# Kernel tuning notes

Measured on AMD Instinct MI355X. Metric: run time of the kernel, lower is better.

## Reference

```python
import jax, jax.numpy as jnp
import numpy as np

D = 1024
S = 2048
B = 4


def setup_inputs() -> dict:
    key = jax.random.key(0)
    ks = jax.random.split(key, 9)
    sc = 1.0 / np.sqrt(D)
    return {
        "x": jax.random.normal(ks[0], (B, S, D), dtype=jnp.float32),
        "Wq": jax.random.normal(ks[1], (D, D), dtype=jnp.float32) * sc,
        "bq": jax.random.normal(ks[2], (D,), dtype=jnp.float32) * 0.02,
        "Wk": jax.random.normal(ks[3], (D, D), dtype=jnp.float32) * sc,
        "bk": jax.random.normal(ks[4], (D,), dtype=jnp.float32) * 0.02,
        "Wv": jax.random.normal(ks[5], (D, D), dtype=jnp.float32) * sc,
        "bv": jax.random.normal(ks[6], (D,), dtype=jnp.float32) * 0.02,
        "Wp": jax.random.normal(ks[7], (D, D), dtype=jnp.float32) * sc,
        "bp": jax.random.normal(ks[8], (D,), dtype=jnp.float32) * 0.02,
    }


def reference(x, Wq, bq, Wk, bk, Wv, bv, Wp, bp):
    # torch nn.Linear: y = x @ W.T + b  (W stored [out, in])
    q = jnp.einsum("bsd,ed->bse", x, Wq) + bq  # [B,S,D]
    k = jnp.einsum("bsd,ed->bse", x, Wk) + bk
    v = jnp.einsum("bsd,ed->bse", x, Wv) + bv

    scale = 1.0 / jnp.sqrt(jnp.asarray(q.shape[-1], q.dtype))
    # single-head attention: contract over full embd_dim (no head split in source)
    scores = jnp.einsum("bqd,bkd->bqk", q, k) * scale  # [B,S,S]

    seq = x.shape[1]
    causal = jnp.tril(jnp.ones((seq, seq), dtype=bool))  # [S,S]
    scores = jnp.where(causal[None, :, :], scores, -jnp.inf)

    attn = jax.nn.softmax(scores, axis=-1)  # [B,S,S]
    out = jnp.einsum("bqk,bkd->bqd", attn, v)  # [B,S,D]
    out = jnp.einsum("bsd,ed->bse", out, Wp) + bp
    return out
```

## Files before the change

### kernel.cpp

```cpp
#include <hip/hip_runtime.h>

#define AS1(p) ((const __attribute__((address_space(1))) void*)(p))
#define AS3(p) ((__attribute__((address_space(3))) void*)(p))

typedef unsigned short u16;
typedef __bf16 bf16x8 __attribute__((ext_vector_type(8)));
typedef short s16x8 __attribute__((ext_vector_type(8)));
typedef float f32x4 __attribute__((ext_vector_type(4)));
typedef unsigned short u16x4 __attribute__((ext_vector_type(4)));
typedef unsigned short u16x8v __attribute__((ext_vector_type(8)));

__device__ __forceinline__ u16 f2bf(float x) {
    unsigned u = __float_as_uint(x);
    unsigned r = (u + 0x7FFFu + ((u >> 16) & 1u)) >> 16;
    return (u16)r;
}
__device__ __forceinline__ float bf2f(u16 x) {
    return __uint_as_float(((unsigned)x) << 16);
}

template <typename V8>
__device__ __forceinline__ auto mfma_sel(V8 a, V8 b, f32x4 c, int)
    -> decltype(__builtin_amdgcn_mfma_f32_16x16x32_bf16(a, b, c, 0, 0, 0))
{
    return __builtin_amdgcn_mfma_f32_16x16x32_bf16(a, b, c, 0, 0, 0);
}
template <typename V8>
__device__ __forceinline__ f32x4 mfma_sel(V8 a, V8 b, f32x4 c, long)
{
    s16x8 a2 = __builtin_bit_cast(s16x8, a);
    s16x8 b2 = __builtin_bit_cast(s16x8, b);
    return __builtin_amdgcn_mfma_f32_16x16x32_bf16(a2, b2, c, 0, 0, 0);
}
__device__ __forceinline__ f32x4 mfma16x16x32(bf16x8 a, bf16x8 b, f32x4 c)
{
    return mfma_sel(a, b, c, 0);
}

__global__ __launch_bounds__(256) void cvt_bf16_kernel(const float* __restrict__ in,
                                                       u16* __restrict__ out, int n4)
{
    int i = blockIdx.x * 256 + threadIdx.x;
    if (i >= n4) return;
    float4 f = ((const float4*)in)[i];
    u16x4 o;
    o.x = f2bf(f.x); o.y = f2bf(f.y); o.z = f2bf(f.z); o.w = f2bf(f.w);
    ((u16x4*)out)[i] = o;
}

__global__ __launch_bounds__(256) void cvt_w4_kernel(const float* __restrict__ Wq,
                                                     const float* __restrict__ Wk,
                                                     const float* __restrict__ Wv,
                                                     const float* __restrict__ Wp,
                                                     u16* __restrict__ Wcat,
                                                     u16* __restrict__ Wpb, int n4)
{
    int i = blockIdx.x * 256 + threadIdx.x;
    if (i >= n4) return;
    const int by = blockIdx.y;
    const float* src = (by == 0) ? Wq : (by == 1) ? Wk : (by == 2) ? Wv : Wp;
    u16* dst = (by == 3) ? Wpb : (Wcat + (size_t)by * n4 * 4);
    float4 f = ((const float4*)src)[i];
    u16x4 o;
    o.x = f2bf(f.x); o.y = f2bf(f.y); o.z = f2bf(f.z); o.w = f2bf(f.w);
    ((u16x4*)dst)[i] = o;
}

__global__ __launch_bounds__(256) void transpose16(const u16* __restrict__ in,
                                                   u16* __restrict__ out, int R, int C)
{
    __shared__ u16 tl[64][65];
    const int tr0 = blockIdx.y * 64, tc0 = blockIdx.x * 64;
    const int t = threadIdx.x;
    const int r = t >> 2, c4 = (t & 3) << 4;

    const u16* src = in + (size_t)(tr0 + r) * C + tc0 + c4;
    u16x8v a0 = *(const u16x8v*)src;
    u16x8v a1 = *(const u16x8v*)(src + 8);
    #pragma unroll
    for (int j = 0; j < 8; ++j) { tl[r][c4 + j] = a0[j]; tl[r][c4 + 8 + j] = a1[j]; }
    __syncthreads();

    u16x8v b0, b1;
    #pragma unroll
    for (int j = 0; j < 8; ++j) { b0[j] = tl[c4 + j][r]; b1[j] = tl[c4 + 8 + j][r]; }
    u16* dst = out + (size_t)(tc0 + r) * R + tr0 + c4;
    *(u16x8v*)dst = b0;
    *(u16x8v*)(dst + 8) = b1;
}

#define GBM 128
#define GBN 256
#define GBK 64
#define ABUF 16384
#define BBUF 32768
#define TBUF (ABUF + BBUF)
#define LDS_NT2 (3 * TBUF)

template <int BIAS, int OUTBF16, int CSKIP, int CKB>
__global__ __launch_bounds__(512, 2)
void gemm_nt2(const u16* __restrict__ A, const u16* __restrict__ B,
              void* __restrict__ Cv, const float* __restrict__ bias,
              void* __restrict__ C2, const float* __restrict__ bias2,
              void* __restrict__ C3, const float* __restrict__ bias3,
              int M, int N, int K, int lda, int ldb, int ldc,
              long long sA, long long sB, long long sC, float scale)
{
    extern __shared__ char smem[];

    int by = blockIdx.y;
    if (CKB) by = gridDim.y - 1 - by;
    const int m0 = by * GBM;
    const int n0 = blockIdx.x * GBN;
    if (CSKIP && n0 > m0 + GBM - 1) return;

    const int z = blockIdx.z;
    A += (size_t)z * (size_t)sA;
    B += (size_t)z * (size_t)sB;

    const int t = threadIdx.x;
    const int lane = t & 63;
    const int w = t >> 6;
    const int wr = w >> 2;
    const int wc = w & 3;
    const int fr = lane & 15, fg = lane >> 4;

    int Keff = K;
    if (CKB) { Keff = m0 + GBM; if (Keff > K) Keff = K; }
    const int nk = Keff / GBK;

    f32x4 acc[4][4] = {};

    auto STAGE = [&](int kt, int buf) {
        const int k0 = kt * GBK;
        char* sb = smem + buf * TBUF;
        #pragma unroll
        for (int i = 0; i < 2; ++i) {
            int c = t + i * 512;
            int row = c >> 3;
            int sl = (c & 7) ^ (row & 7);
            __builtin_amdgcn_global_load_lds(
                AS1(A + (size_t)(m0 + row) * lda + k0 + sl * 8),
                AS3(sb + c * 16), 16, 0, 0);
        }
        #pragma unroll
        for (int i = 0; i < 4; ++i) {
            int c = t + i * 512;
            int row = c >> 3;
            int sl = (c & 7) ^ (row & 7);
            __builtin_amdgcn_global_load_lds(
                AS1(B + (size_t)(n0 + row) * ldb + k0 + sl * 8),
                AS3(sb + ABUF + c * 16), 16, 0, 0);
        }
    };

    STAGE(0, 0);
    STAGE(1, 1);
    asm volatile("s_waitcnt vmcnt(6)" ::: "memory");
    __builtin_amdgcn_s_barrier();

    int cur = 0;
    for (int kt = 0; kt < nk; ++kt) {
        int pb = cur + 2; if (pb >= 3) pb -= 3;
        const bool pf = (kt + 2 < nk);
        if (pf) STAGE(kt + 2, pb);

        const char* la = smem + cur * TBUF;
        const char* lb = la + ABUF;
        #pragma unroll
        for (int kk = 0; kk < GBK; kk += 32) {
            const int cs = (kk >> 3) + fg;
            bf16x8 af[4], bfv[4];
            #pragma unroll
            for (int mi = 0; mi < 4; ++mi) {
                int row = wr * 64 + mi * 16 + fr;
                af[mi] = *(const bf16x8*)(la + (row << 7) + ((cs ^ (row & 7)) << 4));
            }
            #pragma unroll
            for (int ni = 0; ni < 4; ++ni) {
                int row = wc * 64 + ni * 16 + fr;
                bfv[ni] = *(const bf16x8*)(lb + (row << 7) + ((cs ^ (row & 7)) << 4));
            }
            __builtin_amdgcn_s_setprio(1);
            #pragma unroll
            for (int mi = 0; mi < 4; ++mi)
                #pragma unroll
                for (int ni = 0; ni < 4; ++ni)
                    acc[mi][ni] = mfma16x16x32(af[mi], bfv[ni], acc[mi][ni]);
            __builtin_amdgcn_s_setprio(0);
        }

        if (pf) asm volatile("s_waitcnt vmcnt(6)" ::: "memory");
        else    asm volatile("s_waitcnt vmcnt(0)" ::: "memory");
        __builtin_amdgcn_s_barrier();
        ++cur; if (cur >= 3) cur = 0;
    }

    #pragma unroll
    for (int mi = 0; mi < 4; ++mi) {
        #pragma unroll
        for (int ni = 0; ni < 4; ++ni) {
            int col = n0 + wc * 64 + ni * 16 + fr;
            int row0 = m0 + wr * 64 + mi * 16 + fg * 4;
            if (BIAS == 3) {
                int seg = col >> 10;
                int ccol = col & 1023;
                u16* dst = (seg == 0) ? (u16*)Cv : (seg == 1) ? (u16*)C2 : (u16*)C3;
                float b = ((seg == 0) ? bias : (seg == 1) ? bias2 : bias3)[ccol];
                float sc_ = (seg == 0) ? scale : 1.f;
                #pragma unroll
                for (int j = 0; j < 4; ++j)
                    dst[(size_t)(row0 + j) * 1024 + ccol] =
                        f2bf((acc[mi][ni][j] + b) * sc_);
            } else {
                float bval = (BIAS == 1) ? bias[col] : 0.f;
                #pragma unroll
                for (int j = 0; j < 4; ++j) {
                    float v = (acc[mi][ni][j] + bval) * scale;
                    size_t off = (size_t)z * (size_t)sC + (size_t)(row0 + j) * ldc + col;
                    if (OUTBF16) ((u16*)Cv)[off] = f2bf(v);
                    else         ((float*)Cv)[off] = v;
                }
            }
        }
    }
}

__device__ __forceinline__ float waveMax(float v) {
    #pragma unroll
    for (int o = 32; o > 0; o >>= 1) v = fmaxf(v, __shfl_xor(v, o));
    return v;
}
__device__ __forceinline__ float waveSum(float v) {
    #pragma unroll
    for (int o = 32; o > 0; o >>= 1) v += __shfl_xor(v, o);
    return v;
}

__global__ __launch_bounds__(256) void softmax_causal_bf16(u16* __restrict__ scores, int S)
{
    __shared__ float red[4];
    const int gb = blockIdx.x;
    const int b = gb / S;
    const int i = gb - b * S;
    u16* row = scores + (size_t)b * S * S + (size_t)i * S;
    const int t = threadIdx.x;
    const int jlim = ((i >> 7) + 1) << 7;
    const int j0 = t << 3;
    const bool act = j0 < jlim;

    float v[8];
    float mx = -1e30f;
    if (act) {
        u16x8v raw = *(const u16x8v*)(row + j0);
        #pragma unroll
        for (int e = 0; e < 8; ++e) {
            float x = bf2f(raw[e]);
            v[e] = (j0 + e <= i) ? x : -1e30f;
            mx = fmaxf(mx, v[e]);
        }
    } else {
        #pragma unroll
        for (int e = 0; e < 8; ++e) v[e] = -1e30f;
    }

    mx = waveMax(mx);
    const int wv = t >> 6;
    if ((t & 63) == 0) red[wv] = mx;
    __syncthreads();
    mx = fmaxf(fmaxf(red[0], red[1]), fmaxf(red[2], red[3]));
    __syncthreads();

    float sum = 0.f;
    if (act) {
        #pragma unroll
        for (int e = 0; e < 8; ++e) {
            float ex = (v[e] > -1e29f) ? __expf(v[e] - mx) : 0.f;
            v[e] = ex;
            sum += ex;
        }
    }
    sum = waveSum(sum);
    if ((t & 63) == 0) red[wv] = sum;
    __syncthreads();
    sum = red[0] + red[1] + red[2] + red[3];
    const float inv = 1.f / sum;

    if (act) {
        u16x8v o;
        #pragma unroll
        for (int e = 0; e < 8; ++e) o[e] = f2bf(v[e] * inv);
        *(u16x8v*)(row + j0) = o;
    }
}

extern "C" void kernel_launch(void* const* d_in, const int* in_sizes, int n_in,
                              void* d_out, int out_size, void* d_ws, size_t ws_size,
                              hipStream_t stream)
{
    (void)in_sizes; (void)n_in; (void)out_size;
    const float* x  = (const float*)d_in[0];
    const float* Wq = (const float*)d_in[1];
    const float* bq = (const float*)d_in[2];
    const float* Wk = (const float*)d_in[3];
    const float* bk = (const float*)d_in[4];
    const float* Wv = (const float*)d_in[5];
    const float* bv = (const float*)d_in[6];
    const float* Wp = (const float*)d_in[7];
    const float* bp = (const float*)d_in[8];

    const int D = 1024, S = 2048, B = 4;
    const int M = B * S;

    char* p = (char*)d_ws;
    u16* xb   = (u16*)p; p += (size_t)M * D * 2;
    u16* Wcat = (u16*)p; p += (size_t)3 * D * D * 2;
    u16* Wpb  = (u16*)p; p += (size_t)D * D * 2;
    u16* qb   = (u16*)p; p += (size_t)M * D * 2;
    u16* kb   = (u16*)p; p += (size_t)M * D * 2;
    u16* vTb  = (u16*)p; p += (size_t)M * D * 2;
    u16* vb   = (u16*)p;
    u16* sc   = (u16*)p;
    u16* attnb = xb;

    const size_t fixed = (size_t)p - (size_t)d_ws;
    const size_t sb1   = (size_t)S * S * 2;
    const size_t vbsz  = (size_t)M * D * 2;
    int zb = (ws_size >= fixed + (4 * sb1 > vbsz ? 4 * sb1 : vbsz)) ? 4
           : (ws_size >= fixed + (2 * sb1 > vbsz ? 2 * sb1 : vbsz)) ? 2 : 1;

    hipFuncSetAttribute((const void*)gemm_nt2<3, 1, 0, 0>,
                        hipFuncAttributeMaxDynamicSharedMemorySize, LDS_NT2);
    hipFuncSetAttribute((const void*)gemm_nt2<0, 1, 1, 0>,
                        hipFuncAttributeMaxDynamicSharedMemorySize, LDS_NT2);
    hipFuncSetAttribute((const void*)gemm_nt2<0, 1, 0, 1>,
                        hipFuncAttributeMaxDynamicSharedMemorySize, LDS_NT2);
    hipFuncSetAttribute((const void*)gemm_nt2<1, 0, 0, 0>,
                        hipFuncAttributeMaxDynamicSharedMemorySize, LDS_NT2);

    cvt_bf16_kernel<<<(M * D / 4 + 255) / 256, 256, 0, stream>>>(x, xb, M * D / 4);
    cvt_w4_kernel<<<dim3((D * D / 4 + 255) / 256, 4), 256, 0, stream>>>(
        Wq, Wk, Wv, Wp, Wcat, Wpb, D * D / 4);

    gemm_nt2<3, 1, 0, 0><<<dim3(3 * D / GBN, M / GBM, 1), 512, LDS_NT2, stream>>>(
        xb, Wcat, qb, bq, kb, bk, vb, bv,
        M, 3 * D, D, D, D, D, 0, 0, 0, 0.03125f);

    transpose16<<<dim3(D / 64, M / 64), 256, 0, stream>>>(vb, vTb, M, D);

    for (int b0 = 0; b0 < B; b0 += zb) {
        gemm_nt2<0, 1, 1, 0><<<dim3(S / GBN, S / GBM, zb), 512, LDS_NT2, stream>>>(
            qb + (size_t)b0 * S * D, kb + (size_t)b0 * S * D, sc, nullptr,
            nullptr, nullptr, nullptr, nullptr,
            S, S, D, D, D, S,
            (long long)S * D, (long long)S * D, (long long)S * S, 1.0f);
        softmax_causal_bf16<<<zb * S, 256, 0, stream>>>(sc, S);
        gemm_nt2<0, 1, 0, 1><<<dim3(D / GBN, S / GBM, zb), 512, LDS_NT2, stream>>>(
            sc, vTb + (size_t)b0 * S, attnb + (size_t)b0 * S * D, nullptr,
            nullptr, nullptr, nullptr, nullptr,
            S, D, S, S, M, D,
            (long long)S * S, (long long)S, (long long)S * D, 1.0f);
    }

    gemm_nt2<1, 0, 0, 0><<<dim3(D / GBN, M / GBM, 1), 512, LDS_NT2, stream>>>(
        attnb, Wpb, d_out, bp, nullptr, nullptr, nullptr, nullptr,
        M, D, D, D, D, D, 0, 0, 0, 1.0f);
}
```

Before: 200.7 us.

## Add 256x256 double-buffered GEMM for QKV projection and causal scores

Adds a new GEMM kernel with a 256x256 output tile, double-buffered LDS staging and a per-half-K barrier schedule. Each wave holds an 8x4 block of MFMA accumulators, which raises arithmetic intensity per LDS load. The kernel is used for the fused QKV projection and the causal QK^T scores. The causal softmax active-column limit is widened to 256-column granularity to match the larger skip tile. The 128 KB LDS footprint, larger diagonal waste in the causal scores and the coarser grid may cut occupancy and load balance.

New measurement: 200.2 us. About the same (-0.2%).

```diff
diff --git a/kernel.cpp b/kernel.cpp
--- a/kernel.cpp
+++ b/kernel.cpp
@@ -89,30 +89,27 @@
     *(u16x8v*)(dst + 8) = b1;
 }
 
-#define GBM 128
-#define GBN 256
-#define GBK 64
-#define ABUF 16384
-#define BBUF 32768
-#define TBUF (ABUF + BBUF)
-#define LDS_NT2 (3 * TBUF)
-
-template <int BIAS, int OUTBF16, int CSKIP, int CKB>
+#define HBM 256
+#define HBN 256
+#define HBK 64
+#define HABUF 32768
+#define HTBUF 65536
+#define LDS_256 131072
+
+template <int BIAS, int OUTBF16, int CSKIP>
 __global__ __launch_bounds__(512, 2)
-void gemm_nt2(const u16* __restrict__ A, const u16* __restrict__ B,
-              void* __restrict__ Cv, const float* __restrict__ bias,
-              void* __restrict__ C2, const float* __restrict__ bias2,
-              void* __restrict__ C3, const float* __restrict__ bias3,
-              int M, int N, int K, int lda, int ldb, int ldc,
-              long long sA, long long sB, long long sC, float scale)
+void gemm256(const u16* __restrict__ A, const u16* __restrict__ B,
+             void* __restrict__ Cv, const float* __restrict__ bias,
+             void* __restrict__ C2, const float* __restrict__ bias2,
+             void* __restrict__ C3, const float* __restrict__ bias3,
+             int M, int N, int K, int lda, int ldb, int ldc,
+             long long sA, long long sB, long long sC, float scale)
 {
     extern __shared__ char smem[];
 
-    int by = blockIdx.y;
-    if (CKB) by = gridDim.y - 1 - by;
-    const int m0 = by * GBM;
-    const int n0 = blockIdx.x * GBN;
-    if (CSKIP && n0 > m0 + GBM - 1) return;
+    const int m0 = blockIdx.y * HBM;
+    const int n0 = blockIdx.x * HBN;
+    if (CSKIP && n0 > m0 + HBM - 1) return;
 
     const int z = blockIdx.z;
     A += (size_t)z * (size_t)sA;
@@ -125,17 +122,15 @@
     const int wc = w & 3;
     const int fr = lane & 15, fg = lane >> 4;
 
-    int Keff = K;
-    if (CKB) { Keff = m0 + GBM; if (Keff > K) Keff = K; }
-    const int nk = Keff / GBK;
-
-    f32x4 acc[4][4] = {};
+    const int nk = K / HBK;
+
+    f32x4 acc[8][4] = {};
 
     auto STAGE = [&](int kt, int buf) {
-        const int k0 = kt * GBK;
-        char* sb = smem + buf * TBUF;
-        #pragma unroll
-        for (int i = 0; i < 2; ++i) {
+        const int k0 = kt * HBK;
+        char* sb = smem + buf * HTBUF;
+        #pragma unroll
+        for (int i = 0; i < 4; ++i) {
             int c = t + i * 512;
             int row = c >> 3;
             int sl = (c & 7) ^ (row & 7);
@@ -150,30 +145,27 @@
             int sl = (c & 7) ^ (row & 7);
             __builtin_amdgcn_global_load_lds(
                 AS1(B + (size_t)(n0 + row) * ldb + k0 + sl * 8),
-                AS3(sb + ABUF + c * 16), 16, 0, 0);
+                AS3(sb + HABUF + c * 16), 16, 0, 0);
         }
     };
 
     STAGE(0, 0);
-    STAGE(1, 1);
-    asm volatile("s_waitcnt vmcnt(6)" ::: "memory");
+    asm volatile("s_waitcnt vmcnt(0)" ::: "memory");
     __builtin_amdgcn_s_barrier();
 
     int cur = 0;
     for (int kt = 0; kt < nk; ++kt) {
-        int pb = cur + 2; if (pb >= 3) pb -= 3;
-        const bool pf = (kt + 2 < nk);
-        if (pf) STAGE(kt + 2, pb);
-
-        const char* la = smem + cur * TBUF;
-        const char* lb = la + ABUF;
-        #pragma unroll
-        for (int kk = 0; kk < GBK; kk += 32) {
+        const char* la = smem + cur * HTBUF;
+        const char* lb = la + HABUF;
+        const bool pf = (kt + 1 < nk);
+
+        #pragma unroll
+        for (int kk = 0; kk < HBK; kk += 32) {
             const int cs = (kk >> 3) + fg;
-            bf16x8 af[4], bfv[4];
-            #pragma unroll
-            for (int mi = 0; mi < 4; ++mi) {
-                int row = wr * 64 + mi * 16 + fr;
+            bf16x8 af[8], bfv[4];
+            #pragma unroll
+            for (int mi = 0; mi < 8; ++mi) {
+                int row = wr * 128 + mi * 16 + fr;
                 af[mi] = *(const bf16x8*)(la + (row << 7) + ((cs ^ (row & 7)) << 4));
             }
             #pragma unroll
@@ -181,27 +173,30 @@
                 int row = wc * 64 + ni * 16 + fr;
                 bfv[ni] = *(const bf16x8*)(lb + (row << 7) + ((cs ^ (row & 7)) << 4));
             }
+            if (kk == 0 && pf) STAGE(kt + 1, cur ^ 1);
+
+            __builtin_amdgcn_s_barrier();
+            asm volatile("s_waitcnt lgkmcnt(0)" ::: "memory");
             __builtin_amdgcn_s_setprio(1);
             #pragma unroll
-            for (int mi = 0; mi < 4; ++mi)
+            for (int mi = 0; mi < 8; ++mi)
                 #pragma unroll
                 for (int ni = 0; ni < 4; ++ni)
                     acc[mi][ni] = mfma16x16x32(af[mi], bfv[ni], acc[mi][ni]);
             __builtin_amdgcn_s_setprio(0);
-        }
-
-        if (pf) asm volatile("s_waitcnt vmcnt(6)" ::: "memory");
-        else    asm volatile("s_waitcnt vmcnt(0)" ::: "memory");
-        __builtin_amdgcn_s_barrier();
-        ++cur; if (cur >= 3) cur = 0;
-    }
-
-    #pragma unroll
-    for (int mi = 0; mi < 4; ++mi) {
+            if (kk == 32)
+                asm volatile("s_waitcnt vmcnt(0)" ::: "memory");
+            __builtin_amdgcn_s_barrier();
+        }
+        cur ^= 1;
+    }
+
+    #pragma unroll
+    for (int mi = 0; mi < 8; ++mi) {
         #pragma unroll
         for (int ni = 0; ni < 4; ++ni) {
             int col = n0 + wc * 64 + ni * 16 + fr;
-            int row0 = m0 + wr * 64 + mi * 16 + fg * 4;
+            int row0 = m0 + wr * 128 + mi * 16 + fg * 4;
             if (BIAS == 3) {
                 int seg = col >> 10;
                 int ccol = col & 1023;
@@ -226,6 +221,129 @@
     }
 }
 
+#define GBM 128
+#define GBN 256
+#define GBK 64
+#define ABUF 16384
+#define BBUF 32768
+#define TBUF (ABUF + BBUF)
+#define LDS_NT2 (3 * TBUF)
+
+template <int BIAS, int OUTBF16, int CSKIP, int CKB>
+__global__ __launch_bounds__(512, 2)
+void gemm_nt2(const u16* __restrict__ A, const u16* __restrict__ B,
+              void* __restrict__ Cv, const float* __restrict__ bias,
+              int M, int N, int K, int lda, int ldb, int ldc,
+              long long sA, long long sB, long long sC, float scale)
+{
+    extern __shared__ char smem[];
+
+    int by = blockIdx.y;
+    if (CKB) by = gridDim.y - 1 - by;
+    const int m0 = by * GBM;
+    const int n0 = blockIdx.x * GBN;
+    if (CSKIP && n0 > m0 + GBM - 1) return;
+
+    const int z = blockIdx.z;
+    A += (size_t)z * (size_t)sA;
+    B += (size_t)z * (size_t)sB;
+
+    const int t = threadIdx.x;
+    const int lane = t & 63;
+    const int w = t >> 6;
+    const int wr = w >> 2;
+    const int wc = w & 3;
+    const int fr = lane & 15, fg = lane >> 4;
+
+    int Keff = K;
+    if (CKB) { Keff = m0 + GBM; if (Keff > K) Keff = K; }
+    const int nk = Keff / GBK;
+
+    f32x4 acc[4][4] = {};
+
+    auto STAGE = [&](int kt, int buf) {
+        const int k0 = kt * GBK;
+        char* sb = smem + buf * TBUF;
+        #pragma unroll
+        for (int i = 0; i < 2; ++i) {
+            int c = t + i * 512;
+            int row = c >> 3;
+            int sl = (c & 7) ^ (row & 7);
+            __builtin_amdgcn_global_load_lds(
+                AS1(A + (size_t)(m0 + row) * lda + k0 + sl * 8),
+                AS3(sb + c * 16), 16, 0, 0);
+        }
+        #pragma unroll
+        for (int i = 0; i < 4; ++i) {
+            int c = t + i * 512;
+            int row = c >> 3;
+            int sl = (c & 7) ^ (row & 7);
+            __builtin_amdgcn_global_load_lds(
+                AS1(B + (size_t)(n0 + row) * ldb + k0 + sl * 8),
+                AS3(sb + ABUF + c * 16), 16, 0, 0);
+        }
+    };
+
+    STAGE(0, 0);
+    STAGE(1, 1);
+    asm volatile("s_waitcnt vmcnt(6)" ::: "memory");
+    __builtin_amdgcn_s_barrier();
+
+    int cur = 0;
+    for (int kt = 0; kt < nk; ++kt) {
+        int pb = cur + 2; if (pb >= 3) pb -= 3;
+        const bool pf = (kt + 2 < nk);
+        if (pf) STAGE(kt + 2, pb);
+
+        const char* la = smem + cur * TBUF;
+        const char* lb = la + ABUF;
+        #pragma unroll
+        for (int kk = 0; kk < GBK; kk += 32) {
+            const int cs = (kk >> 3) + fg;
+            bf16x8 af[4], bfv[4];
+            #pragma unroll
+            for (int mi = 0; mi < 4; ++mi) {
+                int row = wr * 64 + mi * 16 + fr;
+                af[mi] = *(const bf16x8*)(la + (row << 7) + ((cs ^ (row & 7)) << 4));
+            }
+            #pragma unroll
+            for (int ni = 0; ni < 4; ++ni) {
+                int row = wc * 64 + ni * 16 + fr;
+                bfv[ni] = *(const bf16x8*)(lb + (row << 7) + ((cs ^ (row & 7)) << 4));
+            }
+            __builtin_amdgcn_s_setprio(1);
+            #pragma unroll
+            for (int mi = 0; mi < 4; ++mi)
+                #pragma unroll
+                for (int ni = 0; ni < 4; ++ni)
+                    acc[mi][ni] = mfma16x16x32(af[mi], bfv[ni], acc[mi][ni]);
+            __builtin_amdgcn_s_setprio(0);
+        }
+
+        if (pf) asm volatile("s_waitcnt vmcnt(6)" ::: "memory");
+        else    asm volatile("s_waitcnt vmcnt(0)" ::: "memory");
+        __builtin_amdgcn_s_barrier();
+        ++cur; if (cur >= 3) cur = 0;
+    }
+
+    #pragma unroll
+    for (int mi = 0; mi < 4; ++mi) {
+        #pragma unroll
+        for (int ni = 0; ni < 4; ++ni) {
+            int col = n0 + wc * 64 + ni * 16 + fr;
+            int row0 = m0 + wr * 64 + mi * 16 + fg * 4;
+            float bval = (BIAS == 1) ? bias[col] : 0.f;
+            #pragma unroll
+            for (int j = 0; j < 4; ++j) {
+                float v = (acc[mi][ni][j] + bval) * scale;
+                size_t off = (size_t)z * (size_t)sC + (size_t)(row0 + j) * ldc + col;
+                if (OUTBF16) ((u16*)Cv)[off] = f2bf(v);
+                else         ((float*)Cv)[off] = v;
+            }
+        }
+    }
+}
+
 __device__ __forceinline__ float waveMax(float v) {
     #pragma unroll
     for (int o = 32; o > 0; o >>= 1) v = fmaxf(v, __shfl_xor(v, o));
@@ -245,7 +363,7 @@
     const int i = gb - b * S;
     u16* row = scores + (size_t)b * S * S + (size_t)i * S;
     const int t = threadIdx.x;
-    const int jlim = ((i >> 7) + 1) << 7;
+    const int jlim = ((i >> 8) + 1) << 8;
     const int j0 = t << 3;
     const bool act = j0 < jlim;
 
@@ -329,10 +447,10 @@
     int zb = (ws_size >= fixed + (4 * sb1 > vbsz ? 4 * sb1 : vbsz)) ? 4
            : (ws_size >= fixed + (2 * sb1 > vbsz ? 2 * sb1 : vbsz)) ? 2 : 1;
 
-    hipFuncSetAttribute((const void*)gemm_nt2<3, 1, 0, 0>,
-                        hipFuncAttributeMaxDynamicSharedMemorySize, LDS_NT2);
-    hipFuncSetAttribute((const void*)gemm_nt2<0, 1, 1, 0>,
-                        hipFuncAttributeMaxDynamicSharedMemorySize, LDS_NT2);
+    hipFuncSetAttribute((const void*)gemm256<3, 1, 0>,
+                        hipFuncAttributeMaxDynamicSharedMemorySize, LDS_256);
+    hipFuncSetAttribute((const void*)gemm256<0, 1, 1>,
+                        hipFuncAttributeMaxDynamicSharedMemorySize, LDS_256);
     hipFuncSetAttribute((const void*)gemm_nt2<0, 1, 0, 1>,
                         hipFuncAttributeMaxDynamicSharedMemorySize, LDS_NT2);
     hipFuncSetAttribute((const void*)gemm_nt2<1, 0, 0, 0>,
@@ -342,27 +460,26 @@
     cvt_w4_kernel<<<dim3((D * D / 4 + 255) / 256, 4), 256, 0, stream>>>(
         Wq, Wk, Wv, Wp, Wcat, Wpb, D * D / 4);
 
-    gemm_nt2<3, 1, 0, 0><<<dim3(3 * D / GBN, M / GBM, 1), 512, LDS_NT2, stream>>>(
+    gemm256<3, 1, 0><<<dim3(3 * D / HBN, M / HBM), 512, LDS_256, stream>>>(
         xb, Wcat, qb, bq, kb, bk, vb, bv,
         M, 3 * D, D, D, D, D, 0, 0, 0, 0.03125f);
 
     transpose16<<<dim3(D / 64, M / 64), 256, 0, stream>>>(vb, vTb, M, D);
 
     for (int b0 = 0; b0 < B; b0 += zb) {
-        gemm_nt2<0, 1, 1, 0><<<dim3(S / GBN, S / GBM, zb), 512, LDS_NT2, stream>>>(
+        gemm256<0, 1, 1><<<dim3(S / HBN, S / HBM, zb), 512, LDS_256, stream>>>(
             qb + (size_t)b0 * S * D, kb + (size_t)b0 * S * D, sc, nullptr,
             nullptr, nullptr, nullptr, nullptr,
             S, S, D, D, D, S,
             (long long)S * D, (long long)S * D, (long long)S * S, 1.0f);
         softmax_causal_bf16<<<zb * S, 256, 0, stream>>>(sc, S);
         gemm_nt2<0, 1, 0, 1><<<dim3(D / GBN, S / GBM, zb), 512, LDS_NT2, stream>>>(
-            sc, vTb + (size_t)b0 * S, attnb + (size_t)b0 * S * D, nullptr,
-            nullptr, nullptr, nullptr, nullptr,
+            sc, vTb + (size_t)b0 * S, attnb + (size_t)b0 * S * D,  nullptr,
             S, D, S, S, M, D,
             (long long)S * S, (long long)S, (long long)S * D, 1.0f);
     }
 
     gemm_nt2<1, 0, 0, 0><<<dim3(D / GBN, M / GBM, 1), 512, LDS_NT2, stream>>>(
-        attnb, Wpb, d_out, bp, nullptr, nullptr, nullptr, nullptr,
+        attnb, Wpb, d_out, bp,
         M, D, D, D, D, D, 0, 0, 0, 1.0f);
 }
```

## Replace triple-buffered 128x256 GEMM with single-buffered 128x128 tile kernel

Applied to the files above, without the earlier changes.

Replaces the 512-thread, 128x256-tile GEMM that used a three-stage global_load_lds prefetch pipeline with a 256-thread, 128x128-tile kernel. The new kernel has a single static LDS buffer and synchronises with __syncthreads around each K step. It also adds an optional block-id swizzle for the projection GEMMs, meant to improve L2 locality. Smaller tiles and less LDS per block are meant to give more blocks and higher occupancy, but the change drops load/compute overlap and adds extra barriers per K iteration.

Result: no change. 199.3 us (-0.7%).

```diff
diff --git a/kernel.cpp b/kernel.cpp
--- a/kernel.cpp
+++ b/kernel.cpp
@@ -89,30 +89,33 @@
     *(u16x8v*)(dst + 8) = b1;
 }
 
-#define GBM 128
-#define GBN 256
-#define GBK 64
-#define ABUF 16384
-#define BBUF 32768
-#define TBUF (ABUF + BBUF)
-#define LDS_NT2 (3 * TBUF)
-
-template <int BIAS, int OUTBF16, int CSKIP, int CKB>
-__global__ __launch_bounds__(512, 2)
-void gemm_nt2(const u16* __restrict__ A, const u16* __restrict__ B,
-              void* __restrict__ Cv, const float* __restrict__ bias,
-              void* __restrict__ C2, const float* __restrict__ bias2,
-              void* __restrict__ C3, const float* __restrict__ bias3,
-              int M, int N, int K, int lda, int ldb, int ldc,
-              long long sA, long long sB, long long sC, float scale)
-{
-    extern __shared__ char smem[];
-
-    int by = blockIdx.y;
+#define MBM 128
+#define MBK 64
+
+template <int BIAS, int OUTBF16, int CSKIP, int CKB, int SWZ>
+__global__ __launch_bounds__(256, 3)
+void gemm128(const u16* __restrict__ A, const u16* __restrict__ B,
+             void* __restrict__ Cv, const float* __restrict__ bias,
+             void* __restrict__ C2, const float* __restrict__ bias2,
+             void* __restrict__ C3, const float* __restrict__ bias3,
+             int M, int N, int K, int lda, int ldb, int ldc,
+             long long sA, long long sB, long long sC, float scale)
+{
+    __shared__ u16 lA[MBM * MBK];
+    __shared__ u16 lB[MBM * MBK];
+
+    int bx = blockIdx.x, by = blockIdx.y;
+    if (SWZ) {
+        const int gx = gridDim.x;
+        const int nwg = gx * gridDim.y;
+        int id = by * gx + bx;
+        id = (id & 7) * (nwg >> 3) + (id >> 3);
+        bx = id % gx; by = id / gx;
+    }
     if (CKB) by = gridDim.y - 1 - by;
-    const int m0 = by * GBM;
-    const int n0 = blockIdx.x * GBN;
-    if (CSKIP && n0 > m0 + GBM - 1) return;
+    const int m0 = by * MBM;
+    const int n0 = bx * MBM;
+    if (CSKIP && n0 > m0 + MBM - 1) return;
 
     const int z = blockIdx.z;
     A += (size_t)z * (size_t)sA;
@@ -121,65 +124,45 @@
     const int t = threadIdx.x;
     const int lane = t & 63;
     const int w = t >> 6;
-    const int wr = w >> 2;
-    const int wc = w & 3;
+    const int wr = w >> 1;
+    const int wc = w & 1;
     const int fr = lane & 15, fg = lane >> 4;
 
     int Keff = K;
-    if (CKB) { Keff = m0 + GBM; if (Keff > K) Keff = K; }
-    const int nk = Keff / GBK;
+    if (CKB) { Keff = m0 + MBM; if (Keff > K) Keff = K; }
+    const int nk = Keff / MBK;
 
     f32x4 acc[4][4] = {};
 
-    auto STAGE = [&](int kt, int buf) {
-        const int k0 = kt * GBK;
-        char* sb = smem + buf * TBUF;
-        #pragma unroll
-        for (int i = 0; i < 2; ++i) {
-            int c = t + i * 512;
+    for (int kt = 0; kt < nk; ++kt) {
+        const int k0 = kt * MBK;
+        #pragma unroll
+        for (int i = 0; i < 4; ++i) {
+            int c = t + i * 256;
             int row = c >> 3;
             int sl = (c & 7) ^ (row & 7);
             __builtin_amdgcn_global_load_lds(
                 AS1(A + (size_t)(m0 + row) * lda + k0 + sl * 8),
-                AS3(sb + c * 16), 16, 0, 0);
-        }
-        #pragma unroll
-        for (int i = 0; i < 4; ++i) {
-            int c = t + i * 512;
-            int row = c >> 3;
-            int sl = (c & 7) ^ (row & 7);
+                AS3(&lA[c * 8]), 16, 0, 0);
             __builtin_amdgcn_global_load_lds(
                 AS1(B + (size_t)(n0 + row) * ldb + k0 + sl * 8),
-                AS3(sb + ABUF + c * 16), 16, 0, 0);
-        }
-    };
-
-    STAGE(0, 0);
-    STAGE(1, 1);
-    asm volatile("s_waitcnt vmcnt(6)" ::: "memory");
-    __builtin_amdgcn_s_barrier();
-
-    int cur = 0;
-    for (int kt = 0; kt < nk; ++kt) {
-        int pb = cur + 2; if (pb >= 3) pb -= 3;
-        const bool pf = (kt + 2 < nk);
-        if (pf) STAGE(kt + 2, pb);
-
-        const char* la = smem + cur * TBUF;
-        const char* lb = la + ABUF;
-        #pragma unroll
-        for (int kk = 0; kk < GBK; kk += 32) {
+                AS3(&lB[c * 8]), 16, 0, 0);
+        }
+        __syncthreads();
+
+        #pragma unroll
+        for (int kk = 0; kk < MBK; kk += 32) {
             const int cs = (kk >> 3) + fg;
             bf16x8 af[4], bfv[4];
             #pragma unroll
             for (int mi = 0; mi < 4; ++mi) {
                 int row = wr * 64 + mi * 16 + fr;
-                af[mi] = *(const bf16x8*)(la + (row << 7) + ((cs ^ (row & 7)) << 4));
+                af[mi] = *(const bf16x8*)&lA[row * 64 + ((cs ^ (row & 7)) << 3)];
             }
             #pragma unroll
             for (int ni = 0; ni < 4; ++ni) {
                 int row = wc * 64 + ni * 16 + fr;
-                bfv[ni] = *(const bf16x8*)(lb + (row << 7) + ((cs ^ (row & 7)) << 4));
+                bfv[ni] = *(const bf16x8*)&lB[row * 64 + ((cs ^ (row & 7)) << 3)];
             }
             __builtin_amdgcn_s_setprio(1);
             #pragma unroll
@@ -189,11 +172,7 @@
                     acc[mi][ni] = mfma16x16x32(af[mi], bfv[ni], acc[mi][ni]);
             __builtin_amdgcn_s_setprio(0);
         }
-
-        if (pf) asm volatile("s_waitcnt vmcnt(6)" ::: "memory");
-        else    asm volatile("s_waitcnt vmcnt(0)" ::: "memory");
-        __builtin_amdgcn_s_barrier();
-        ++cur; if (cur >= 3) cur = 0;
+        __syncthreads();
     }
 
     #pragma unroll
@@ -329,40 +308,31 @@
     int zb = (ws_size >= fixed + (4 * sb1 > vbsz ? 4 * sb1 : vbsz)) ? 4
            : (ws_size >= fixed + (2 * sb1 > vbsz ? 2 * sb1 : vbsz)) ? 2 : 1;
 
-    hipFuncSetAttribute((const void*)gemm_nt2<3, 1, 0, 0>,
-                        hipFuncAttributeMaxDynamicSharedMemorySize, LDS_NT2);
-    hipFuncSetAttribute((const void*)gemm_nt2<0, 1, 1, 0>,
-                        hipFuncAttributeMaxDynamicSharedMemorySize, LDS_NT2);
-    hipFuncSetAttribute((const void*)gemm_nt2<0, 1, 0, 1>,
-                        hipFuncAttributeMaxDynamicSharedMemorySize, LDS_NT2);
-    hipFuncSetAttribute((const void*)gemm_nt2<1, 0, 0, 0>,
-                        hipFuncAttributeMaxDynamicSharedMemorySize, LDS_NT2);
-
     cvt_bf16_kernel<<<(M * D / 4 + 255) / 256, 256, 0, stream>>>(x, xb, M * D / 4);
     cvt_w4_kernel<<<dim3((D * D / 4 + 255) / 256, 4), 256, 0, stream>>>(
         Wq, Wk, Wv, Wp, Wcat, Wpb, D * D / 4);
 
-    gemm_nt2<3, 1, 0, 0><<<dim3(3 * D / GBN, M / GBM, 1), 512, LDS_NT2, stream>>>(
+    gemm128<3, 1, 0, 0, 1><<<dim3(3 * D / MBM, M / MBM), 256, 0, stream>>>(
         xb, Wcat, qb, bq, kb, bk, vb, bv,
         M, 3 * D, D, D, D, D, 0, 0, 0, 0.03125f);
 
     transpose16<<<dim3(D / 64, M / 64), 256, 0, stream>>>(vb, vTb, M, D);
 
     for (int b0 = 0; b0 < B; b0 += zb) {
-        gemm_nt2<0, 1, 1, 0><<<dim3(S / GBN, S / GBM, zb), 512, LDS_NT2, stream>>>(
+        gemm128<0, 1, 1, 0, 0><<<dim3(S / MBM, S / MBM, zb), 256, 0, stream>>>(
             qb + (size_t)b0 * S * D, kb + (size_t)b0 * S * D, sc, nullptr,
             nullptr, nullptr, nullptr, nullptr,
             S, S, D, D, D, S,
             (long long)S * D, (long long)S * D, (long long)S * S, 1.0f);
         softmax_causal_bf16<<<zb * S, 256, 0, stream>>>(sc, S);
-        gemm_nt2<0, 1, 0, 1><<<dim3(D / GBN, S / GBM, zb), 512, LDS_NT2, stream>>>(
+        gemm128<0, 1, 0, 1, 0><<<dim3(D / MBM, S / MBM, zb), 256, 0, stream>>>(
             sc, vTb + (size_t)b0 * S, attnb + (size_t)b0 * S * D, nullptr,
             nullptr, nullptr, nullptr, nullptr,
             S, D, S, S, M, D,
             (long long)S * S, (long long)S, (long long)S * D, 1.0f);
     }
 
-    gemm_nt2<1, 0, 0, 0><<<dim3(D / GBN, M / GBM, 1), 512, LDS_NT2, stream>>>(
+    gemm128<1, 0, 0, 0, 1><<<dim3(D / MBM, M / MBM), 256, 0, stream>>>(
         attnb, Wpb, d_out, bp, nullptr, nullptr, nullptr, nullptr,
         M, D, D, D, D, D, 0, 0, 0, 1.0f);
 }
```
